# Kernel tuning notes

Measured on AMD Instinct MI355X. Metric: run time of the kernel, lower is better.

## Reference

```python
import jax, jax.numpy as jnp
import numpy as np

B, NM, D, H = 16384, 5, 256, 8
LN_EPS = 1e-5


def _ln(x, g, b):
    m = jnp.mean(x, axis=-1, keepdims=True)
    v = jnp.var(x, axis=-1, keepdims=True)
    return (x - m) / jnp.sqrt(v + LN_EPS) * g + b


def _mha(q_in, kv_in, Wi, bi, Wo, bo):
    # q_in: [B,1,D], kv_in: [B,1,D]; Wi: [3D,D] packed q/k/v like nn.MultiheadAttention
    Bq, Lq, Dm = q_in.shape
    Lk = kv_in.shape[1]
    dh = Dm // H
    q = (q_in @ Wi[:Dm].T + bi[:Dm]).reshape(Bq, Lq, H, dh).transpose(0, 2, 1, 3)
    k = (kv_in @ Wi[Dm:2 * Dm].T + bi[Dm:2 * Dm]).reshape(Bq, Lk, H, dh).transpose(0, 2, 1, 3)
    v = (kv_in @ Wi[2 * Dm:].T + bi[2 * Dm:]).reshape(Bq, Lk, H, dh).transpose(0, 2, 1, 3)
    scores = jnp.einsum('bhqd,bhkd->bhqk', q, k) * (1.0 / np.sqrt(dh))
    attn = jax.nn.softmax(scores, axis=-1)  # trivially 1.0 for Lk=1, kept for fidelity
    out = jnp.einsum('bhqk,bhkd->bhqd', attn, v).transpose(0, 2, 1, 3).reshape(Bq, Lq, Dm)
    return out @ Wo.T + bo


def setup_inputs() -> dict:
    key = jax.random.key(0)
    ks = jax.random.split(key, 8)
    s = 0.02
    return {
        'x': jax.random.normal(ks[0], (B, NM, D), jnp.float32),
        'self_Wi': jax.random.normal(ks[1], (3 * D, D), jnp.float32) * s,
        'self_bi': jnp.zeros((3 * D,), jnp.float32),
        'self_Wo': jax.random.normal(ks[2], (D, D), jnp.float32) * s,
        'self_bo': jnp.zeros((D,), jnp.float32),
        'cross_Wi': jax.random.normal(ks[3], (4, 3 * D, D), jnp.float32) * s,
        'cross_bi': jnp.zeros((4, 3 * D), jnp.float32),
        'cross_Wo': jax.random.normal(ks[4], (4, D, D), jnp.float32) * s,
        'cross_bo': jnp.zeros((4, D), jnp.float32),
        'cross_ln_g': jnp.ones((4, D), jnp.float32),
        'cross_ln_b': jnp.zeros((4, D), jnp.float32),
        'gate_ln_g': jnp.ones((D,), jnp.float32),
        'gate_ln_b': jnp.zeros((D,), jnp.float32),
        'gate_W': jax.random.normal(ks[5], (NM, D), jnp.float32) * s,
        'gate_b': jnp.zeros((NM,), jnp.float32),
        'final_ln_g': jnp.ones((D,), jnp.float32),
        'final_ln_b': jnp.zeros((D,), jnp.float32),
        'modal_idx': 2,
    }


def reference(x, self_Wi, self_bi, self_Wo, self_bo,
              cross_Wi, cross_bi, cross_Wo, cross_bo, cross_ln_g, cross_ln_b,
              gate_ln_g, gate_ln_b, gate_W, gate_b, final_ln_g, final_ln_b,
              modal_idx):
    query = x[:, modal_idx:modal_idx + 1, :]  # [B,1,D]
    self_out = _mha(query, query, self_Wi, self_bi, self_Wo, self_bo)

    other_idx = [i for i in range(NM) if i != modal_idx]
    kv = jnp.swapaxes(x[:, other_idx, :], 0, 1)[:, :, None, :]  # [4,B,1,D]

    def branch(Wi, bi, Wo, bo, g, b, kv_i):
        a = _mha(query, kv_i, Wi, bi, Wo, bo)
        return _ln(query + a, g, b)  # dropout is identity in eval

    cross_outs = jax.vmap(branch)(cross_Wi, cross_bi, cross_Wo, cross_bo,
                                  cross_ln_g, cross_ln_b, kv)  # [4,B,1,D]

    gates = jax.nn.softmax(_ln(query, gate_ln_g, gate_ln_b) @ gate_W.T + gate_b, axis=-1)  # [B,1,5]
    combined = gates[..., 0:1] * self_out + jnp.einsum('nbld,bln->bld', cross_outs, gates[..., 1:])
    return _ln(query + combined, final_ln_g, final_ln_b)
```

## Files before the change

kernel.cpp:

```cpp
#include <hip/hip_runtime.h>


typedef __attribute__((ext_vector_type(8))) short short8;
typedef __attribute__((ext_vector_type(4))) float floatx4;

__device__ __forceinline__ float b2f(unsigned short h) {
    union { unsigned int u; float f; } v; v.u = ((unsigned int)h) << 16; return v.f;
}
__device__ __forceinline__ unsigned short f2b(float f) {
    union { unsigned int u; float f; } v; v.f = f;
    unsigned int u = v.u;
    return (unsigned short)((u + 0x7FFFu + ((u >> 16) & 1u)) >> 16);
}

__global__ __launch_bounds__(256) void k_fuse(
    const float* __restrict__ sWi, const float* __restrict__ sbi,
    const float* __restrict__ sWo, const float* __restrict__ sbo,
    const float* __restrict__ cWi, const float* __restrict__ cbi,
    const float* __restrict__ cWo, const float* __restrict__ cbo,
    unsigned short* __restrict__ WF, float* __restrict__ BF)
{
    int s = blockIdx.y;
    int i0 = blockIdx.x * 4;
    int tid = threadIdx.x;
    const float *Wo, *Wv, *bv, *bo;
    if (s == 0) { Wo = sWo; Wv = sWi + 512 * 256; bv = sbi + 512; bo = sbo; }
    else {
        int n = s - 1;
        Wo = cWo + n * 65536;
        Wv = cWi + n * 768 * 256 + 512 * 256;
        bv = cbi + n * 768 + 512;
        bo = cbo + n * 256;
    }
    __shared__ float wo[4 * 256];
    #pragma unroll
    for (int it = 0; it < 4; ++it) {
        int idx = tid + it * 256;
        wo[idx] = Wo[i0 * 256 + idx];
    }
    __syncthreads();
    float a0 = 0.f, a1 = 0.f, a2 = 0.f, a3 = 0.f;
    for (int k = 0; k < 256; ++k) {
        float wv = Wv[k * 256 + tid];
        a0 += wo[k] * wv;
        a1 += wo[256 + k] * wv;
        a2 += wo[512 + k] * wv;
        a3 += wo[768 + k] * wv;
    }
    unsigned short* dst = WF + ((size_t)s * 256 + i0) * 256 + tid;
    dst[0] = f2b(a0); dst[256] = f2b(a1); dst[512] = f2b(a2); dst[768] = f2b(a3);
    if (tid < 4) {
        int i = i0 + tid;
        float bacc = 0.f;
        for (int k = 0; k < 256; ++k) bacc += Wo[i * 256 + k] * bv[k];
        BF[s * 256 + i] = bacc + bo[i];
    }
}

__device__ __forceinline__ float wred(float v) {
    #pragma unroll
    for (int o = 32; o > 0; o >>= 1) v += __shfl_xor(v, o, 64);
    return v;
}

__global__ __launch_bounds__(512, 4) void k_main(
    const float* __restrict__ x, const unsigned short* __restrict__ WF,
    const float* __restrict__ BF,
    const float* __restrict__ cln_g, const float* __restrict__ cln_b,
    const float* __restrict__ gln_g, const float* __restrict__ gln_b,
    const float* __restrict__ gW, const float* __restrict__ gb,
    const float* __restrict__ fln_g, const float* __restrict__ fln_b,
    const int* __restrict__ midx, float* __restrict__ out)
{
    __shared__ __align__(16) unsigned short A[32 * 264];
    __shared__ __align__(16) unsigned short Yb[32 * 264];
    __shared__ float gWs[5 * 256];
    __shared__ float gLDS[32 * 8];

    int m = midx[0];
    int b0 = blockIdx.x * 32;
    int tid = threadIdx.x;
    int wave = tid >> 6, lane = tid & 63;
    int l16 = lane & 15, q4 = lane >> 4;
    int j = lane * 4;

    gWs[tid] = gW[tid];
    gWs[tid + 512] = gW[tid + 512];
    if (tid < 256) gWs[tid + 1024] = gW[tid + 1024];

    float qv[4][4];
    #pragma unroll
    for (int rr = 0; rr < 4; ++rr) {
        int r = wave * 4 + rr;
        float4 u = *(const float4*)(x + ((size_t)(b0 + r) * 5 + m) * 256 + j);
        qv[rr][0] = u.x; qv[rr][1] = u.y; qv[rr][2] = u.z; qv[rr][3] = u.w;
    }
    float4 glg = *(const float4*)(gln_g + j);
    float4 glb = *(const float4*)(gln_b + j);
    float gbv[5];
    #pragma unroll
    for (int n = 0; n < 5; ++n) gbv[n] = gb[n];

    __syncthreads();

    #pragma unroll
    for (int rr = 0; rr < 4; ++rr) {
        int r = wave * 4 + rr;
        float s1 = wred(qv[rr][0] + qv[rr][1] + qv[rr][2] + qv[rr][3]);
        float s2 = wred(qv[rr][0]*qv[rr][0] + qv[rr][1]*qv[rr][1] +
                        qv[rr][2]*qv[rr][2] + qv[rr][3]*qv[rr][3]);
        float mn = s1 * (1.f / 256.f);
        float vr = s2 * (1.f / 256.f) - mn * mn;
        float rs = rsqrtf(vr + 1e-5f);
        float qln[4];
        qln[0] = (qv[rr][0] - mn) * rs * glg.x + glb.x;
        qln[1] = (qv[rr][1] - mn) * rs * glg.y + glb.y;
        qln[2] = (qv[rr][2] - mn) * rs * glg.z + glb.z;
        qln[3] = (qv[rr][3] - mn) * rs * glg.w + glb.w;
        float g[5];
        #pragma unroll
        for (int n = 0; n < 5; ++n) {
            float p = qln[0] * gWs[n * 256 + j] + qln[1] * gWs[n * 256 + j + 1]
                    + qln[2] * gWs[n * 256 + j + 2] + qln[3] * gWs[n * 256 + j + 3];
            g[n] = wred(p) + gbv[n];
        }
        float mx = g[0];
        #pragma unroll
        for (int n = 1; n < 5; ++n) mx = fmaxf(mx, g[n]);
        float es = 0.f;
        #pragma unroll
        for (int n = 0; n < 5; ++n) { g[n] = __expf(g[n] - mx); es += g[n]; }
        float inv = 1.f / es;
        if (lane == 0) {
            #pragma unroll
            for (int n = 0; n < 5; ++n) gLDS[r * 8 + n] = g[n] * inv;
        }
    }

    float comb[4][4];
    #pragma unroll
    for (int rr = 0; rr < 4; ++rr)
        #pragma unroll
        for (int i = 0; i < 4; ++i) comb[rr][i] = 0.f;

    for (int s = 0; s < 5; ++s) {
        int mod = (s == 0) ? m : ((s - 1 < m) ? s - 1 : s);
        #pragma unroll
        for (int it = 0; it < 4; ++it) {
            int c = tid + it * 512;
            int row = c >> 6;
            int c4 = (c & 63) << 2;
            float4 v = *(const float4*)(x + ((size_t)(b0 + row) * 5 + mod) * 256 + c4);
            uint2 p;
            p.x = (unsigned int)f2b(v.x) | ((unsigned int)f2b(v.y) << 16);
            p.y = (unsigned int)f2b(v.z) | ((unsigned int)f2b(v.w) << 16);
            *(uint2*)(&A[row * 264 + c4]) = p;
        }
        __syncthreads();

        floatx4 acc[2][2];
        #pragma unroll
        for (int rt = 0; rt < 2; ++rt)
            #pragma unroll
            for (int ct = 0; ct < 2; ++ct) acc[rt][ct] = (floatx4){0.f, 0.f, 0.f, 0.f};
        const unsigned short* wB = WF + (size_t)s * 65536;
        #pragma unroll
        for (int kk = 0; kk < 8; ++kk) {
            int k = kk * 32 + q4 * 8;
            short8 a0 = *(const short8*)(&A[l16 * 264 + k]);
            short8 a1 = *(const short8*)(&A[(16 + l16) * 264 + k]);
            short8 bb[2];
            #pragma unroll
            for (int ct = 0; ct < 2; ++ct)
                bb[ct] = *(const short8*)(wB + (size_t)(wave * 32 + ct * 16 + l16) * 256 + k);
            #pragma unroll
            for (int ct = 0; ct < 2; ++ct) {
                acc[0][ct] = __builtin_amdgcn_mfma_f32_16x16x32_bf16(a0, bb[ct], acc[0][ct], 0, 0, 0);
                acc[1][ct] = __builtin_amdgcn_mfma_f32_16x16x32_bf16(a1, bb[ct], acc[1][ct], 0, 0, 0);
            }
        }
        #pragma unroll
        for (int rt = 0; rt < 2; ++rt)
            #pragma unroll
            for (int i = 0; i < 4; ++i) {
                int r = rt * 16 + q4 * 4 + i;
                #pragma unroll
                for (int ct = 0; ct < 2; ++ct)
                    Yb[r * 264 + wave * 32 + ct * 16 + l16] = f2b(acc[rt][ct][i]);
            }
        __syncthreads();

        float4 bfv = *(const float4*)(BF + s * 256 + j);
        if (s == 0) {
            #pragma unroll
            for (int rr = 0; rr < 4; ++rr) {
                int r = wave * 4 + rr;
                uint2 u = *(const uint2*)(&Yb[r * 264 + j]);
                float y0 = b2f(u.x & 0xffff) + bfv.x, y1 = b2f(u.x >> 16) + bfv.y;
                float y2 = b2f(u.y & 0xffff) + bfv.z, y3 = b2f(u.y >> 16) + bfv.w;
                float g0 = gLDS[r * 8 + 0];
                comb[rr][0] += g0 * y0; comb[rr][1] += g0 * y1;
                comb[rr][2] += g0 * y2; comb[rr][3] += g0 * y3;
            }
        } else {
            float4 cg = *(const float4*)(cln_g + (s - 1) * 256 + j);
            float4 cb = *(const float4*)(cln_b + (s - 1) * 256 + j);
            #pragma unroll
            for (int rr = 0; rr < 4; ++rr) {
                int r = wave * 4 + rr;
                uint2 u = *(const uint2*)(&Yb[r * 264 + j]);
                float t0 = qv[rr][0] + b2f(u.x & 0xffff) + bfv.x;
                float t1 = qv[rr][1] + b2f(u.x >> 16)    + bfv.y;
                float t2 = qv[rr][2] + b2f(u.y & 0xffff) + bfv.z;
                float t3 = qv[rr][3] + b2f(u.y >> 16)    + bfv.w;
                float s1 = wred(t0 + t1 + t2 + t3);
                float s2 = wred(t0*t0 + t1*t1 + t2*t2 + t3*t3);
                float mn = s1 * (1.f / 256.f);
                float vr = s2 * (1.f / 256.f) - mn * mn;
                float rs = rsqrtf(vr + 1e-5f);
                float gs = gLDS[r * 8 + s];
                comb[rr][0] += gs * ((t0 - mn) * rs * cg.x + cb.x);
                comb[rr][1] += gs * ((t1 - mn) * rs * cg.y + cb.y);
                comb[rr][2] += gs * ((t2 - mn) * rs * cg.z + cb.z);
                comb[rr][3] += gs * ((t3 - mn) * rs * cg.w + cb.w);
            }
        }
    }

    float4 fg = *(const float4*)(fln_g + j);
    float4 fb = *(const float4*)(fln_b + j);
    #pragma unroll
    for (int rr = 0; rr < 4; ++rr) {
        int r = wave * 4 + rr;
        float t0 = qv[rr][0] + comb[rr][0], t1 = qv[rr][1] + comb[rr][1];
        float t2 = qv[rr][2] + comb[rr][2], t3 = qv[rr][3] + comb[rr][3];
        float s1 = wred(t0 + t1 + t2 + t3);
        float s2 = wred(t0*t0 + t1*t1 + t2*t2 + t3*t3);
        float mn = s1 * (1.f / 256.f);
        float vr = s2 * (1.f / 256.f) - mn * mn;
        float rs = rsqrtf(vr + 1e-5f);
        float4 ov;
        ov.x = (t0 - mn) * rs * fg.x + fb.x;
        ov.y = (t1 - mn) * rs * fg.y + fb.y;
        ov.z = (t2 - mn) * rs * fg.z + fb.z;
        ov.w = (t3 - mn) * rs * fg.w + fb.w;
        *(float4*)(out + (size_t)(b0 + r) * 256 + j) = ov;
    }
}

extern "C" void kernel_launch(void* const* d_in, const int* in_sizes, int n_in,
                              void* d_out, int out_size, void* d_ws, size_t ws_size,
                              hipStream_t stream) {
    const float* x    = (const float*)d_in[0];
    const float* sWi  = (const float*)d_in[1];
    const float* sbi  = (const float*)d_in[2];
    const float* sWo  = (const float*)d_in[3];
    const float* sbo  = (const float*)d_in[4];
    const float* cWi  = (const float*)d_in[5];
    const float* cbi  = (const float*)d_in[6];
    const float* cWo  = (const float*)d_in[7];
    const float* cbo  = (const float*)d_in[8];
    const float* clng = (const float*)d_in[9];
    const float* clnb = (const float*)d_in[10];
    const float* glng = (const float*)d_in[11];
    const float* glnb = (const float*)d_in[12];
    const float* gW   = (const float*)d_in[13];
    const float* gb   = (const float*)d_in[14];
    const float* flng = (const float*)d_in[15];
    const float* flnb = (const float*)d_in[16];
    const int* midx   = (const int*)d_in[17];
    float* out        = (float*)d_out;

    char* ws = (char*)d_ws;
    unsigned short* WF = (unsigned short*)ws;
    float* BF          = (float*)(ws + 655360);

    k_fuse<<<dim3(64, 5), 256, 0, stream>>>(sWi, sbi, sWo, sbo, cWi, cbi, cWo, cbo, WF, BF);
    k_main<<<512, 512, 0, stream>>>(x, WF, BF, clng, clnb, glng, glnb, gW, gb, flng, flnb, midx, out);
}
```

Before: 224.9 us.

## Shrink main kernel tiles to 16 rows, 256 threads, and parallelize fused bias

```diff
diff --git a/kernel.cpp b/kernel.cpp
--- a/kernel.cpp
+++ b/kernel.cpp
@@ -40,6 +40,7 @@
     }
     __syncthreads();
     float a0 = 0.f, a1 = 0.f, a2 = 0.f, a3 = 0.f;
+    #pragma unroll 8
     for (int k = 0; k < 256; ++k) {
         float wv = Wv[k * 256 + tid];
         a0 += wo[k] * wv;
@@ -49,12 +50,16 @@
     }
     unsigned short* dst = WF + ((size_t)s * 256 + i0) * 256 + tid;
     dst[0] = f2b(a0); dst[256] = f2b(a1); dst[512] = f2b(a2); dst[768] = f2b(a3);
-    if (tid < 4) {
-        int i = i0 + tid;
-        float bacc = 0.f;
-        for (int k = 0; k < 256; ++k) bacc += Wo[i * 256 + k] * bv[k];
-        BF[s * 256 + i] = bacc + bo[i];
-    }
+    int wv_ = tid >> 6, ln = tid & 63;
+    float p = 0.f;
+    #pragma unroll
+    for (int u = 0; u < 4; ++u) {
+        int k = ln * 4 + u;
+        p += wo[wv_ * 256 + k] * bv[k];
+    }
+    #pragma unroll
+    for (int o = 32; o > 0; o >>= 1) p += __shfl_xor(p, o, 64);
+    if (ln == 0) BF[s * 256 + i0 + wv_] = p + bo[i0 + wv_];
 }
 
 __device__ __forceinline__ float wred(float v) {
@@ -63,7 +68,7 @@
     return v;
 }
 
-__global__ __launch_bounds__(512, 4) void k_main(
+__global__ __launch_bounds__(256, 6) void k_main(
     const float* __restrict__ x, const unsigned short* __restrict__ WF,
     const float* __restrict__ BF,
     const float* __restrict__ cln_g, const float* __restrict__ cln_b,
@@ -72,21 +77,16 @@
     const float* __restrict__ fln_g, const float* __restrict__ fln_b,
     const int* __restrict__ midx, float* __restrict__ out)
 {
-    __shared__ __align__(16) unsigned short A[32 * 264];
-    __shared__ __align__(16) unsigned short Yb[32 * 264];
-    __shared__ float gWs[5 * 256];
-    __shared__ float gLDS[32 * 8];
-
-    int m = midx[0];
-    int b0 = blockIdx.x * 32;
-    int tid = threadIdx.x;
-    int wave = tid >> 6, lane = tid & 63;
-    int l16 = lane & 15, q4 = lane >> 4;
-    int j = lane * 4;
-
-    gWs[tid] = gW[tid];
-    gWs[tid + 512] = gW[tid + 512];
-    if (tid < 256) gWs[tid + 1024] = gW[tid + 1024];
+    __shared__ __align__(16) unsigned short A[16 * 264];
+    __shared__ __align__(16) unsigned short Yb[16 * 264];
+    __shared__ float gLDS[16 * 8];
+
+    const int m = midx[0];
+    const int b0 = blockIdx.x * 16;
+    const int tid = threadIdx.x;
+    const int wave = tid >> 6, lane = tid & 63;
+    const int l16 = lane & 15, q4 = lane >> 4;
+    const int j = lane * 4;
 
     float qv[4][4];
     #pragma unroll
@@ -100,8 +100,6 @@
     float gbv[5];
     #pragma unroll
     for (int n = 0; n < 5; ++n) gbv[n] = gb[n];
-
-    __syncthreads();
 
     #pragma unroll
     for (int rr = 0; rr < 4; ++rr) {
@@ -120,8 +118,8 @@
         float g[5];
         #pragma unroll
         for (int n = 0; n < 5; ++n) {
-            float p = qln[0] * gWs[n * 256 + j] + qln[1] * gWs[n * 256 + j + 1]
-                    + qln[2] * gWs[n * 256 + j + 2] + qln[3] * gWs[n * 256 + j + 3];
+            float4 w4 = *(const float4*)(gW + n * 256 + j);
+            float p = qln[0] * w4.x + qln[1] * w4.y + qln[2] * w4.z + qln[3] * w4.w;
             g[n] = wred(p) + gbv[n];
         }
         float mx = g[0];
@@ -147,7 +145,7 @@
         int mod = (s == 0) ? m : ((s - 1 < m) ? s - 1 : s);
         #pragma unroll
         for (int it = 0; it < 4; ++it) {
-            int c = tid + it * 512;
+            int c = tid + it * 256;
             int row = c >> 6;
             int c4 = (c & 63) << 2;
             float4 v = *(const float4*)(x + ((size_t)(b0 + row) * 5 + mod) * 256 + c4);
@@ -158,36 +156,27 @@
         }
         __syncthreads();
 
-        floatx4 acc[2][2];
-        #pragma unroll
-        for (int rt = 0; rt < 2; ++rt)
-            #pragma unroll
-            for (int ct = 0; ct < 2; ++ct) acc[rt][ct] = (floatx4){0.f, 0.f, 0.f, 0.f};
+        floatx4 acc[4];
+        #pragma unroll
+        for (int ct = 0; ct < 4; ++ct) acc[ct] = (floatx4){0.f, 0.f, 0.f, 0.f};
         const unsigned short* wB = WF + (size_t)s * 65536;
         #pragma unroll
         for (int kk = 0; kk < 8; ++kk) {
             int k = kk * 32 + q4 * 8;
-            short8 a0 = *(const short8*)(&A[l16 * 264 + k]);
-            short8 a1 = *(const short8*)(&A[(16 + l16) * 264 + k]);
-            short8 bb[2];
-            #pragma unroll
-            for (int ct = 0; ct < 2; ++ct)
-                bb[ct] = *(const short8*)(wB + (size_t)(wave * 32 + ct * 16 + l16) * 256 + k);
-            #pragma unroll
-            for (int ct = 0; ct < 2; ++ct) {
-                acc[0][ct] = __builtin_amdgcn_mfma_f32_16x16x32_bf16(a0, bb[ct], acc[0][ct], 0, 0, 0);
-                acc[1][ct] = __builtin_amdgcn_mfma_f32_16x16x32_bf16(a1, bb[ct], acc[1][ct], 0, 0, 0);
+            short8 a = *(const short8*)(&A[l16 * 264 + k]);
+            #pragma unroll
+            for (int ct = 0; ct < 4; ++ct) {
+                short8 bb = *(const short8*)(wB + (size_t)(wave * 64 + ct * 16 + l16) * 256 + k);
+                acc[ct] = __builtin_amdgcn_mfma_f32_16x16x32_bf16(a, bb, acc[ct], 0, 0, 0);
             }
         }
         #pragma unroll
-        for (int rt = 0; rt < 2; ++rt)
-            #pragma unroll
-            for (int i = 0; i < 4; ++i) {
-                int r = rt * 16 + q4 * 4 + i;
-                #pragma unroll
-                for (int ct = 0; ct < 2; ++ct)
-                    Yb[r * 264 + wave * 32 + ct * 16 + l16] = f2b(acc[rt][ct][i]);
-            }
+        for (int i = 0; i < 4; ++i) {
+            int r = q4 * 4 + i;
+            #pragma unroll
+            for (int ct = 0; ct < 4; ++ct)
+                Yb[r * 264 + wave * 64 + ct * 16 + l16] = f2b(acc[ct][i]);
+        }
         __syncthreads();
 
         float4 bfv = *(const float4*)(BF + s * 256 + j);
@@ -276,5 +265,5 @@
     float* BF          = (float*)(ws + 655360);
 
     k_fuse<<<dim3(64, 5), 256, 0, stream>>>(sWi, sbi, sWo, sbo, cWi, cbi, cWo, cbo, WF, BF);
-    k_main<<<512, 512, 0, stream>>>(x, WF, BF, clng, clnb, glng, glnb, gW, gb, flng, flnb, midx, out);
-}
+    k_main<<<1024, 256, 0, stream>>>(x, WF, BF, clng, clnb, glng, glnb, gW, gb, flng, flnb, midx, out);
+}
```

After: 284.7 us. 1.27x slower.

## Double-buffer modality tile in LDS with register prefetch overlapping MFMA

Applied to the files above, without the earlier changes.

```diff
diff --git a/kernel.cpp b/kernel.cpp
--- a/kernel.cpp
+++ b/kernel.cpp
@@ -72,7 +72,7 @@
     const float* __restrict__ fln_g, const float* __restrict__ fln_b,
     const int* __restrict__ midx, float* __restrict__ out)
 {
-    __shared__ __align__(16) unsigned short A[32 * 264];
+    __shared__ __align__(16) unsigned short Ab[2][32 * 264];
     __shared__ __align__(16) unsigned short Yb[32 * 264];
     __shared__ float gWs[5 * 256];
     __shared__ float gLDS[32 * 8];
@@ -87,6 +87,20 @@
     gWs[tid] = gW[tid];
     gWs[tid + 512] = gW[tid + 512];
     if (tid < 256) gWs[tid + 1024] = gW[tid + 1024];
+
+    {
+        #pragma unroll
+        for (int it = 0; it < 4; ++it) {
+            int c = tid + it * 512;
+            int row = c >> 6;
+            int c4 = (c & 63) << 2;
+            float4 v = *(const float4*)(x + ((size_t)(b0 + row) * 5 + m) * 256 + c4);
+            uint2 p;
+            p.x = (unsigned int)f2b(v.x) | ((unsigned int)f2b(v.y) << 16);
+            p.y = (unsigned int)f2b(v.z) | ((unsigned int)f2b(v.w) << 16);
+            *(uint2*)(&Ab[0][row * 264 + c4]) = p;
+        }
+    }
 
     float qv[4][4];
     #pragma unroll
@@ -143,20 +157,23 @@
         #pragma unroll
         for (int i = 0; i < 4; ++i) comb[rr][i] = 0.f;
 
+    int cur = 0;
     for (int s = 0; s < 5; ++s) {
-        int mod = (s == 0) ? m : ((s - 1 < m) ? s - 1 : s);
-        #pragma unroll
-        for (int it = 0; it < 4; ++it) {
-            int c = tid + it * 512;
-            int row = c >> 6;
-            int c4 = (c & 63) << 2;
-            float4 v = *(const float4*)(x + ((size_t)(b0 + row) * 5 + mod) * 256 + c4);
-            uint2 p;
-            p.x = (unsigned int)f2b(v.x) | ((unsigned int)f2b(v.y) << 16);
-            p.y = (unsigned int)f2b(v.z) | ((unsigned int)f2b(v.w) << 16);
-            *(uint2*)(&A[row * 264 + c4]) = p;
-        }
-        __syncthreads();
+        float4 nreg[4];
+        if (s < 4) {
+            int nmod = (s < m) ? s : s + 1;
+            #pragma unroll
+            for (int it = 0; it < 4; ++it) {
+                int c = tid + it * 512;
+                nreg[it] = *(const float4*)(x + ((size_t)(b0 + (c >> 6)) * 5 + nmod) * 256 + ((c & 63) << 2));
+            }
+        }
+        float4 bfv = *(const float4*)(BF + s * 256 + j);
+        float4 cg, cb;
+        if (s > 0) {
+            cg = *(const float4*)(cln_g + (s - 1) * 256 + j);
+            cb = *(const float4*)(cln_b + (s - 1) * 256 + j);
+        }
 
         floatx4 acc[2][2];
         #pragma unroll
@@ -167,8 +184,8 @@
         #pragma unroll
         for (int kk = 0; kk < 8; ++kk) {
             int k = kk * 32 + q4 * 8;
-            short8 a0 = *(const short8*)(&A[l16 * 264 + k]);
-            short8 a1 = *(const short8*)(&A[(16 + l16) * 264 + k]);
+            short8 a0 = *(const short8*)(&Ab[cur][l16 * 264 + k]);
+            short8 a1 = *(const short8*)(&Ab[cur][(16 + l16) * 264 + k]);
             short8 bb[2];
             #pragma unroll
             for (int ct = 0; ct < 2; ++ct)
@@ -188,9 +205,19 @@
                 for (int ct = 0; ct < 2; ++ct)
                     Yb[r * 264 + wave * 32 + ct * 16 + l16] = f2b(acc[rt][ct][i]);
             }
+        if (s < 4) {
+            #pragma unroll
+            for (int it = 0; it < 4; ++it) {
+                int c = tid + it * 512;
+                float4 v = nreg[it];
+                uint2 p;
+                p.x = (unsigned int)f2b(v.x) | ((unsigned int)f2b(v.y) << 16);
+                p.y = (unsigned int)f2b(v.z) | ((unsigned int)f2b(v.w) << 16);
+                *(uint2*)(&Ab[cur ^ 1][(c >> 6) * 264 + ((c & 63) << 2)]) = p;
+            }
+        }
         __syncthreads();
 
-        float4 bfv = *(const float4*)(BF + s * 256 + j);
         if (s == 0) {
             #pragma unroll
             for (int rr = 0; rr < 4; ++rr) {
@@ -203,8 +230,6 @@
                 comb[rr][2] += g0 * y2; comb[rr][3] += g0 * y3;
             }
         } else {
-            float4 cg = *(const float4*)(cln_g + (s - 1) * 256 + j);
-            float4 cb = *(const float4*)(cln_b + (s - 1) * 256 + j);
             #pragma unroll
             for (int rr = 0; rr < 4; ++rr) {
                 int r = wave * 4 + rr;
@@ -225,6 +250,8 @@
                 comb[rr][3] += gs * ((t3 - mn) * rs * cg.w + cb.w);
             }
         }
+        __syncthreads();
+        cur ^= 1;
     }
 
     float4 fg = *(const float4*)(fln_g + j);
```

Measured after the change: 228.6 us. No clear change (+1.6%).

## Pre-swizzle fused weights into MFMA fragment order and batch B-operand loads

Applied to the files above, without the earlier changes.

```diff
diff --git a/kernel.cpp b/kernel.cpp
--- a/kernel.cpp
+++ b/kernel.cpp
@@ -18,7 +18,7 @@
     const float* __restrict__ sWo, const float* __restrict__ sbo,
     const float* __restrict__ cWi, const float* __restrict__ cbi,
     const float* __restrict__ cWo, const float* __restrict__ cbo,
-    unsigned short* __restrict__ WF, float* __restrict__ BF)
+    unsigned short* __restrict__ WT, float* __restrict__ BF)
 {
     int s = blockIdx.y;
     int i0 = blockIdx.x * 4;
@@ -47,8 +47,17 @@
         a2 += wo[512 + k] * wv;
         a3 += wo[768 + k] * wv;
     }
-    unsigned short* dst = WF + ((size_t)s * 256 + i0) * 256 + tid;
-    dst[0] = f2b(a0); dst[256] = f2b(a1); dst[512] = f2b(a2); dst[768] = f2b(a3);
+    {
+        unsigned short vals[4] = { f2b(a0), f2b(a1), f2b(a2), f2b(a3) };
+        int kk = tid >> 5, q4k = (tid >> 3) & 3, e = tid & 7;
+        #pragma unroll
+        for (int r = 0; r < 4; ++r) {
+            int n = i0 + r;
+            int w = n >> 5, ct = (n >> 4) & 1, l16n = n & 15;
+            size_t idx = (((((((size_t)s * 8 + kk) * 8 + w) * 2 + ct) * 4 + q4k) * 16 + l16n) * 8) + e;
+            WT[idx] = vals[r];
+        }
+    }
     if (tid < 4) {
         int i = i0 + tid;
         float bacc = 0.f;
@@ -64,7 +73,7 @@
 }
 
 __global__ __launch_bounds__(512, 4) void k_main(
-    const float* __restrict__ x, const unsigned short* __restrict__ WF,
+    const float* __restrict__ x, const unsigned short* __restrict__ WT,
     const float* __restrict__ BF,
     const float* __restrict__ cln_g, const float* __restrict__ cln_b,
     const float* __restrict__ gln_g, const float* __restrict__ gln_b,
@@ -163,20 +172,27 @@
         for (int rt = 0; rt < 2; ++rt)
             #pragma unroll
             for (int ct = 0; ct < 2; ++ct) acc[rt][ct] = (floatx4){0.f, 0.f, 0.f, 0.f};
-        const unsigned short* wB = WF + (size_t)s * 65536;
-        #pragma unroll
-        for (int kk = 0; kk < 8; ++kk) {
-            int k = kk * 32 + q4 * 8;
-            short8 a0 = *(const short8*)(&A[l16 * 264 + k]);
-            short8 a1 = *(const short8*)(&A[(16 + l16) * 264 + k]);
-            short8 bb[2];
-            #pragma unroll
-            for (int ct = 0; ct < 2; ++ct)
-                bb[ct] = *(const short8*)(wB + (size_t)(wave * 32 + ct * 16 + l16) * 256 + k);
-            #pragma unroll
-            for (int ct = 0; ct < 2; ++ct) {
-                acc[0][ct] = __builtin_amdgcn_mfma_f32_16x16x32_bf16(a0, bb[ct], acc[0][ct], 0, 0, 0);
-                acc[1][ct] = __builtin_amdgcn_mfma_f32_16x16x32_bf16(a1, bb[ct], acc[1][ct], 0, 0, 0);
+        const unsigned short* wT = WT + (size_t)s * 65536;
+        #pragma unroll
+        for (int h = 0; h < 2; ++h) {
+            short8 bb[8];
+            #pragma unroll
+            for (int kk = 0; kk < 4; ++kk) {
+                int kkg = h * 4 + kk;
+                #pragma unroll
+                for (int ct = 0; ct < 2; ++ct)
+                    bb[kk * 2 + ct] = *(const short8*)(
+                        wT + (((((size_t)kkg * 8 + wave) * 2 + ct) * 4 + q4) * 16 + l16) * 8);
+            }
+            #pragma unroll
+            for (int kk = 0; kk < 4; ++kk) {
+                int k = (h * 4 + kk) * 32 + q4 * 8;
+                short8 a0 = *(const short8*)(&A[l16 * 264 + k]);
+                short8 a1 = *(const short8*)(&A[(16 + l16) * 264 + k]);
+                acc[0][0] = __builtin_amdgcn_mfma_f32_16x16x32_bf16(a0, bb[kk*2+0], acc[0][0], 0, 0, 0);
+                acc[0][1] = __builtin_amdgcn_mfma_f32_16x16x32_bf16(a0, bb[kk*2+1], acc[0][1], 0, 0, 0);
+                acc[1][0] = __builtin_amdgcn_mfma_f32_16x16x32_bf16(a1, bb[kk*2+0], acc[1][0], 0, 0, 0);
+                acc[1][1] = __builtin_amdgcn_mfma_f32_16x16x32_bf16(a1, bb[kk*2+1], acc[1][1], 0, 0, 0);
             }
         }
         #pragma unroll
@@ -272,9 +288,9 @@
     float* out        = (float*)d_out;
 
     char* ws = (char*)d_ws;
-    unsigned short* WF = (unsigned short*)ws;
+    unsigned short* WT = (unsigned short*)ws;
     float* BF          = (float*)(ws + 655360);
 
-    k_fuse<<<dim3(64, 5), 256, 0, stream>>>(sWi, sbi, sWo, sbo, cWi, cbi, cWo, cbo, WF, BF);
-    k_main<<<512, 512, 0, stream>>>(x, WF, BF, clng, clnb, glng, glnb, gW, gb, flng, flnb, midx, out);
-}
+    k_fuse<<<dim3(64, 5), 256, 0, stream>>>(sWi, sbi, sWo, sbo, cWi, cbi, cWo, cbo, WT, BF);
+    k_main<<<512, 512, 0, stream>>>(x, WT, BF, clng, clnb, glng, glnb, gW, gb, flng, flnb, midx, out);
+}
```

Result: faster. 212.8 us (-5.4%).
